# Optimization experiments

Measured on AMD Instinct MI355X. Metric: run time of the kernel, lower is better.

Reference implementation:

```python
import jax, jax.numpy as jnp
import numpy as np

B, L, D, V, O = 512, 256, 256, 100000, 1000  # L must equal D (see MaxPool1d(kernel_size=D) + squeeze)


def setup_inputs() -> dict:
    key = jax.random.key(0)
    k1, k2, k3, k4, k5 = jax.random.split(key, 5)
    input_sentence = jax.random.randint(k1, (B, L), 0, V)
    emb_weight = jax.random.normal(k2, (V, D), dtype=jnp.float32) * 0.02
    # xavier_uniform for W_b: bound = sqrt(6/(D+D))
    bound = float(np.sqrt(6.0 / (D + D)))
    W_b = jax.random.uniform(k3, (D, D), dtype=jnp.float32, minval=-bound, maxval=bound)
    lw = float(np.sqrt(1.0 / D))
    lin_w = jax.random.uniform(k4, (O, D), dtype=jnp.float32, minval=-lw, maxval=lw)
    lin_b = jax.random.uniform(k5, (O,), dtype=jnp.float32, minval=-lw, maxval=lw)
    return {"input_sentence": input_sentence, "emb_weight": emb_weight,
            "W_b": W_b, "lin_w": lin_w, "lin_b": lin_b}


def reference(input_sentence, emb_weight, W_b, lin_w, lin_b):
    # Embedding lookup: [B, L, D]
    we = emb_weight[input_sentence]
    # torch stores embeddings as [B, D, L] then re-transposes inside the co-attention;
    # net effect: C = tanh(E W_b E^T) with E = [B, L, D]  ->  C: [B, L, L]
    C = jnp.tanh(jnp.einsum('bld,de,bme->blm', we, W_b, we))
    # Dropout(p=0.5) is identity in eval mode.
    # MaxPool1d(kernel_size=D) over last axis with L == D -> max over last dim, keepdims
    max_cow = jnp.max(C, axis=-1, keepdims=True)          # [B, L, 1]
    a_q = jax.nn.softmax(max_cow, axis=1)                  # softmax over L
    # bmm(a_q^T [B,1,L], E [B,L,D]) -> [B,1,D], then squeeze dim 1
    f_w = jnp.einsum('blo,bld->bod', a_q, we)[:, 0, :]     # [B, D]
    return f_w @ lin_w.T + lin_b                           # [B, O]
```

## Files before the change

kernel.cpp:

```cpp
#include <hip/hip_runtime.h>
#include <hip/hip_bf16.h>
#include <math.h>

#define B_ 512
#define L_ 256
#define D_ 256
#define V_ 100000
#define O_ 1000

typedef __attribute__((ext_vector_type(8))) short short8;
typedef __attribute__((ext_vector_type(4))) float f32x4;

static __device__ __forceinline__ unsigned short f2bf(float f) {
    union { float f; unsigned u; } v; v.f = f;
    unsigned r = v.u + 0x7FFFu + ((v.u >> 16) & 1u);
    return (unsigned short)(r >> 16);
}
static __device__ __forceinline__ float bf2f(unsigned short u) {
    union { unsigned u; float f; } v; v.u = ((unsigned)u) << 16;
    return v.f;
}
static __device__ __forceinline__ short8 pack8(float4 a, float4 c) {
    short8 o;
    o[0] = (short)f2bf(a.x); o[1] = (short)f2bf(a.y);
    o[2] = (short)f2bf(a.z); o[3] = (short)f2bf(a.w);
    o[4] = (short)f2bf(c.x); o[5] = (short)f2bf(c.y);
    o[6] = (short)f2bf(c.z); o[7] = (short)f2bf(c.w);
    return o;
}
static __device__ __forceinline__ int fsw(int d) { return d ^ (((d >> 5) & 7) << 2); }

__global__ __launch_bounds__(256) void k_wt(const float* __restrict__ Wb,
                                            unsigned short* __restrict__ Wbf) {
    int i = blockIdx.x * 256 + threadIdx.x;
    Wbf[i] = f2bf(Wb[i]);
}

__global__ __launch_bounds__(1024, 4) void k_attn(const int* __restrict__ tok,
                                                  const float* __restrict__ emb,
                                                  const unsigned short* __restrict__ Wbf,
                                                  float* __restrict__ fw) {
    __shared__ __align__(16) char lds[163840];
    char* EsC = lds;
    float* red2    = (float*)(lds + 131072);
    float* scratch = (float*)(lds + 132096);
    float* fred    = (float*)(lds + 132160);

    int b = blockIdx.x;
    int tid = threadIdx.x;
    int wid = tid >> 6, ln = tid & 63;
    int l16 = ln & 15, gp = ln >> 4;
    bool prod = (wid < 8);
    int i0 = (prod ? wid : (wid - 8)) * 32;
    const int* tb = tok + (b << 8);

#pragma unroll
    for (int it = 0; it < 2; it++) {
        int c = it * 1024 + tid;
        int row = c >> 5, c16 = c & 31;
        const float4* src = (const float4*)(emb + ((size_t)tb[row] << 8) + (c16 << 3));
        short8 o = pack8(src[0], src[1]);
        *(short8*)(EsC + ((row << 9) | ((c16 << 4) ^ ((row & 7) << 4)))) = o;
    }

    short8 afr[8][2];
    if (prod) {
#pragma unroll
        for (int k = 0; k < 8; k++)
#pragma unroll
            for (int rf = 0; rf < 2; rf++)
                afr[k][rf] = *(const short8*)(Wbf + ((i0 + rf * 16 + l16) << 8) + k * 32 + gp * 8);
    }
    __syncthreads();

    float rmax[8];
#pragma unroll
    for (int i = 0; i < 8; i++) rmax[i] = -1e30f;

    auto P1strip = [&](int s, char* HtW) {
        f32x4 acc[2][2] = {};
#pragma unroll
        for (int k0 = 0; k0 < 256; k0 += 32) {
            int kk2 = (k0 + gp * 8) * 2;
            short8 b1[2];
#pragma unroll
            for (int cf = 0; cf < 2; cf++) {
                int jg = s * 32 + cf * 16 + l16;
                b1[cf] = *(const short8*)(EsC + ((jg << 9) | (kk2 ^ ((jg & 7) << 4))));
            }
            int ks = k0 >> 5;
            __builtin_amdgcn_s_setprio(1);
#pragma unroll
            for (int rf = 0; rf < 2; rf++)
#pragma unroll
                for (int cf = 0; cf < 2; cf++)
                    acc[rf][cf] = __builtin_amdgcn_mfma_f32_16x16x32_bf16(
                        afr[ks][rf], b1[cf], acc[rf][cf], 0, 0, 0);
            __builtin_amdgcn_s_setprio(0);
        }
#pragma unroll
        for (int rf = 0; rf < 2; rf++)
#pragma unroll
            for (int cf = 0; cf < 2; cf++) {
                int i = i0 + rf * 16 + gp * 4;
                int jl = cf * 16 + l16;
                unsigned long long pk;
                unsigned short* p = (unsigned short*)&pk;
                p[0] = f2bf(acc[rf][cf][0]);
                p[1] = f2bf(acc[rf][cf][1]);
                p[2] = f2bf(acc[rf][cf][2]);
                p[3] = f2bf(acc[rf][cf][3]);
                *(unsigned long long*)(HtW + ((jl << 9) | ((i * 2) ^ ((jl & 7) << 4)))) = pk;
            }
    };

    auto P2strip = [&](char* HtR) {
        f32x4 acc[2][2] = {};
#pragma unroll
        for (int k0 = 0; k0 < 256; k0 += 32) {
            int kk2 = (k0 + gp * 8) * 2;
            short8 b2[2];
#pragma unroll
            for (int cf = 0; cf < 2; cf++) {
                int m = cf * 16 + l16;
                b2[cf] = *(const short8*)(HtR + ((m << 9) | (kk2 ^ ((m & 7) << 4))));
            }
            int ks = k0 >> 5;
            __builtin_amdgcn_s_setprio(1);
#pragma unroll
            for (int rf = 0; rf < 2; rf++)
#pragma unroll
                for (int cf = 0; cf < 2; cf++)
                    acc[rf][cf] = __builtin_amdgcn_mfma_f32_16x16x32_bf16(
                        afr[ks][rf], b2[cf], acc[rf][cf], 0, 0, 0);
            __builtin_amdgcn_s_setprio(0);
        }
#pragma unroll
        for (int rf = 0; rf < 2; rf++)
#pragma unroll
            for (int r = 0; r < 4; r++)
                rmax[rf * 4 + r] = fmaxf(rmax[rf * 4 + r],
                                         fmaxf(acc[rf][0][r], acc[rf][1][r]));
    };

    if (prod) {
        P1strip(0, lds + 131072);
    } else {
        int t4 = tid - 512;
#pragma unroll 2
        for (int it = 0; it < 12; it++) {
            int c = it * 512 + t4;
            int row = 64 + (c >> 5), c16 = c & 31;
            const float4* src = (const float4*)(emb + ((size_t)tb[row] << 8) + (c16 << 3));
            short8 o = pack8(src[0], src[1]);
            *(short8*)(EsC + ((row << 9) | ((c16 << 4) ^ ((row & 7) << 4)))) = o;
        }
    }
    __syncthreads();

    if (!prod) {
#pragma unroll
        for (int k = 0; k < 8; k++)
#pragma unroll
            for (int rf = 0; rf < 2; rf++) {
                int l = i0 + rf * 16 + l16;
                afr[k][rf] = *(const short8*)(EsC +
                    ((l << 9) | ((k * 64 + gp * 16) ^ ((l & 7) << 4))));
            }
    }

    for (int s = 1; s < 8; s++) {
        if (prod) P1strip(s, lds + 131072 + ((s & 1) << 14));
        else      P2strip(lds + 131072 + (((s - 1) & 1) << 14));
        __syncthreads();
    }
    if (!prod) {
        P2strip(lds + 131072 + (1 << 14));
#pragma unroll
        for (int i = 0; i < 8; i++) {
            float v = rmax[i];
            v = fmaxf(v, __shfl_xor(v, 1));
            v = fmaxf(v, __shfl_xor(v, 2));
            v = fmaxf(v, __shfl_xor(v, 4));
            v = fmaxf(v, __shfl_xor(v, 8));
            rmax[i] = v;
        }
        if (l16 == 0) {
#pragma unroll
            for (int rf = 0; rf < 2; rf++)
#pragma unroll
                for (int r = 0; r < 4; r++)
                    red2[i0 + rf * 16 + gp * 4 + r] = rmax[rf * 4 + r];
        }
    }
    __syncthreads();

    float x = -1e30f;
    if (tid < 256) x = tanhf(red2[tid]);
    float mx = x;
#pragma unroll
    for (int s = 1; s < 64; s <<= 1) mx = fmaxf(mx, __shfl_xor(mx, s));
    if (ln == 0 && wid < 4) scratch[wid] = mx;
    __syncthreads();
    float bm = fmaxf(fmaxf(scratch[0], scratch[1]), fmaxf(scratch[2], scratch[3]));
    float e = (tid < 256) ? expf(x - bm) : 0.f;
    float sm = e;
#pragma unroll
    for (int s = 1; s < 64; s <<= 1) sm += __shfl_xor(sm, s);
    if (ln == 0 && wid < 4) scratch[8 + wid] = sm;
    __syncthreads();
    float tot = (scratch[8] + scratch[9]) + (scratch[10] + scratch[11]);
    if (tid < 256) red2[tid] = e / tot;
    __syncthreads();

    if (tid < 512) {
        int g = tid >> 5;
        int d0 = (tid & 31) << 3;
        float s0[8] = {0.f, 0.f, 0.f, 0.f, 0.f, 0.f, 0.f, 0.f};
        int lbase = g << 4;
#pragma unroll
        for (int li = 0; li < 16; li++) {
            int l = lbase + li;
            float aql = red2[l];
            int byt = (l << 9) | ((d0 * 2) ^ ((l & 7) << 4));
            short8 v = *(const short8*)(EsC + byt);
#pragma unroll
            for (int jj = 0; jj < 8; jj++)
                s0[jj] += aql * bf2f((unsigned short)v[jj]);
        }
        f32x4 w0, w1;
        w0[0] = s0[0]; w0[1] = s0[1]; w0[2] = s0[2]; w0[3] = s0[3];
        w1[0] = s0[4]; w1[1] = s0[5]; w1[2] = s0[6]; w1[3] = s0[7];
        *(f32x4*)(fred + g * 256 + fsw(d0)) = w0;
        *(f32x4*)(fred + g * 256 + fsw(d0 + 4)) = w1;
    }
    __syncthreads();
    if (tid < 256) {
        float f = 0.f;
        int dw = fsw(tid);
#pragma unroll
        for (int g2 = 0; g2 < 16; g2++) f += fred[g2 * 256 + dw];
        fw[(b << 8) + tid] = f;
    }
}

__global__ __launch_bounds__(256) void k_out(const float* __restrict__ fw,
                                             const float* __restrict__ lw,
                                             const float* __restrict__ lb,
                                             float* __restrict__ out) {
    __shared__ float As[32][68];
    __shared__ float Bs[64][65];
    int tid = threadIdx.x;
    int tx = tid & 15, ty = tid >> 4;
    int r0 = blockIdx.y * 32, n0 = blockIdx.x * 64;
    float acc[2][4] = {};
    for (int k0 = 0; k0 < 256; k0 += 64) {
        __syncthreads();
#pragma unroll
        for (int it = 0; it < 2; it++) {
            int idx = it * 256 + tid;
            int i = idx >> 4, k4 = (idx & 15) << 2;
            *(float4*)&As[i][k4] = *(const float4*)&fw[(r0 + i) * 256 + k0 + k4];
        }
#pragma unroll
        for (int it = 0; it < 4; it++) {
            int idx = it * 256 + tid;
            int n = idx >> 4, k4 = (idx & 15) << 2;
            int nn = n0 + n;
            float4 v = {0.f, 0.f, 0.f, 0.f};
            if (nn < O_) v = *(const float4*)&lw[(size_t)nn * 256 + k0 + k4];
            Bs[k4][n] = v.x; Bs[k4 + 1][n] = v.y; Bs[k4 + 2][n] = v.z; Bs[k4 + 3][n] = v.w;
        }
        __syncthreads();
#pragma unroll
        for (int k = 0; k < 64; k++) {
            float a0 = As[ty * 2][k], a1 = As[ty * 2 + 1][k];
            float b0 = Bs[k][tx * 4], b1 = Bs[k][tx * 4 + 1];
            float b2 = Bs[k][tx * 4 + 2], b3 = Bs[k][tx * 4 + 3];
            acc[0][0] += a0 * b0; acc[0][1] += a0 * b1; acc[0][2] += a0 * b2; acc[0][3] += a0 * b3;
            acc[1][0] += a1 * b0; acc[1][1] += a1 * b1; acc[1][2] += a1 * b2; acc[1][3] += a1 * b3;
        }
    }
#pragma unroll
    for (int i = 0; i < 2; i++)
#pragma unroll
        for (int j = 0; j < 4; j++) {
            int n = n0 + tx * 4 + j;
            if (n < O_) out[(size_t)(r0 + ty * 2 + i) * O_ + n] = acc[i][j] + lb[n];
        }
}

extern "C" void kernel_launch(void* const* d_in, const int* in_sizes, int n_in,
                              void* d_out, int out_size, void* d_ws, size_t ws_size,
                              hipStream_t stream) {
    const int* tok = (const int*)d_in[0];
    const float* emb = (const float*)d_in[1];
    const float* Wb = (const float*)d_in[2];
    const float* lw = (const float*)d_in[3];
    const float* lb = (const float*)d_in[4];
    float* out = (float*)d_out;

    char* ws = (char*)d_ws;
    unsigned short* Wbf = (unsigned short*)(ws);
    float*          fwp = (float*)(ws + 131072);

    hipLaunchKernelGGL(k_wt,   dim3(256),    dim3(256),  0, stream, Wb, Wbf);
    hipLaunchKernelGGL(k_attn, dim3(512),    dim3(1024), 0, stream, tok, emb, Wbf, fwp);
    hipLaunchKernelGGL(k_out,  dim3(16, 16), dim3(256),  0, stream, fwp, lw, lb, out);
}
```

Measured before the change: 81.26 us.

## Halve attention block to 512 threads with 64-row warps; load full K in output GEMM

```diff
diff --git a/kernel.cpp b/kernel.cpp
--- a/kernel.cpp
+++ b/kernel.cpp
@@ -36,10 +36,10 @@
     Wbf[i] = f2bf(Wb[i]);
 }
 
-__global__ __launch_bounds__(1024, 4) void k_attn(const int* __restrict__ tok,
-                                                  const float* __restrict__ emb,
-                                                  const unsigned short* __restrict__ Wbf,
-                                                  float* __restrict__ fw) {
+__global__ __launch_bounds__(512) void k_attn(const int* __restrict__ tok,
+                                              const float* __restrict__ emb,
+                                              const unsigned short* __restrict__ Wbf,
+                                              float* __restrict__ fw) {
     __shared__ __align__(16) char lds[163840];
     char* EsC = lds;
     float* red2    = (float*)(lds + 131072);
@@ -50,72 +50,35 @@
     int tid = threadIdx.x;
     int wid = tid >> 6, ln = tid & 63;
     int l16 = ln & 15, gp = ln >> 4;
-    bool prod = (wid < 8);
-    int i0 = (prod ? wid : (wid - 8)) * 32;
+    bool prod = (wid < 4);
+    int i0 = (prod ? wid : (wid - 4)) * 64;
     const int* tb = tok + (b << 8);
 
 #pragma unroll
-    for (int it = 0; it < 2; it++) {
-        int c = it * 1024 + tid;
+    for (int it = 0; it < 4; it++) {
+        int c = it * 512 + tid;
         int row = c >> 5, c16 = c & 31;
         const float4* src = (const float4*)(emb + ((size_t)tb[row] << 8) + (c16 << 3));
         short8 o = pack8(src[0], src[1]);
         *(short8*)(EsC + ((row << 9) | ((c16 << 4) ^ ((row & 7) << 4)))) = o;
     }
-
-    short8 afr[8][2];
+    __syncthreads();
+
+    short8 afr[8][4];
     if (prod) {
 #pragma unroll
         for (int k = 0; k < 8; k++)
 #pragma unroll
-            for (int rf = 0; rf < 2; rf++)
+            for (int rf = 0; rf < 4; rf++)
                 afr[k][rf] = *(const short8*)(Wbf + ((i0 + rf * 16 + l16) << 8) + k * 32 + gp * 8);
     }
-    __syncthreads();
-
-    float rmax[8];
-#pragma unroll
-    for (int i = 0; i < 8; i++) rmax[i] = -1e30f;
-
-    auto P1strip = [&](int s, char* HtW) {
-        f32x4 acc[2][2] = {};
-#pragma unroll
-        for (int k0 = 0; k0 < 256; k0 += 32) {
-            int kk2 = (k0 + gp * 8) * 2;
-            short8 b1[2];
-#pragma unroll
-            for (int cf = 0; cf < 2; cf++) {
-                int jg = s * 32 + cf * 16 + l16;
-                b1[cf] = *(const short8*)(EsC + ((jg << 9) | (kk2 ^ ((jg & 7) << 4))));
-            }
-            int ks = k0 >> 5;
-            __builtin_amdgcn_s_setprio(1);
-#pragma unroll
-            for (int rf = 0; rf < 2; rf++)
-#pragma unroll
-                for (int cf = 0; cf < 2; cf++)
-                    acc[rf][cf] = __builtin_amdgcn_mfma_f32_16x16x32_bf16(
-                        afr[ks][rf], b1[cf], acc[rf][cf], 0, 0, 0);
-            __builtin_amdgcn_s_setprio(0);
-        }
-#pragma unroll
-        for (int rf = 0; rf < 2; rf++)
-#pragma unroll
-            for (int cf = 0; cf < 2; cf++) {
-                int i = i0 + rf * 16 + gp * 4;
-                int jl = cf * 16 + l16;
-                unsigned long long pk;
-                unsigned short* p = (unsigned short*)&pk;
-                p[0] = f2bf(acc[rf][cf][0]);
-                p[1] = f2bf(acc[rf][cf][1]);
-                p[2] = f2bf(acc[rf][cf][2]);
-                p[3] = f2bf(acc[rf][cf][3]);
-                *(unsigned long long*)(HtW + ((jl << 9) | ((i * 2) ^ ((jl & 7) << 4)))) = pk;
-            }
-    };
-
-    auto P2strip = [&](char* HtR) {
-        f32x4 acc[2][2] = {};
+
+    float rmax[16];
+#pragma unroll
+    for (int i = 0; i < 16; i++) rmax[i] = -1e30f;
+
+    auto P2body = [&](char* HtR) {
+        f32x4 acc[4][2] = {};
 #pragma unroll
         for (int k0 = 0; k0 < 256; k0 += 32) {
             int kk2 = (k0 + gp * 8) * 2;
@@ -128,7 +91,7 @@
             int ks = k0 >> 5;
             __builtin_amdgcn_s_setprio(1);
 #pragma unroll
-            for (int rf = 0; rf < 2; rf++)
+            for (int rf = 0; rf < 4; rf++)
 #pragma unroll
                 for (int cf = 0; cf < 2; cf++)
                     acc[rf][cf] = __builtin_amdgcn_mfma_f32_16x16x32_bf16(
@@ -136,48 +99,82 @@
             __builtin_amdgcn_s_setprio(0);
         }
 #pragma unroll
-        for (int rf = 0; rf < 2; rf++)
+        for (int rf = 0; rf < 4; rf++)
 #pragma unroll
             for (int r = 0; r < 4; r++)
                 rmax[rf * 4 + r] = fmaxf(rmax[rf * 4 + r],
                                          fmaxf(acc[rf][0][r], acc[rf][1][r]));
     };
 
-    if (prod) {
-        P1strip(0, lds + 131072);
-    } else {
-        int t4 = tid - 512;
-#pragma unroll 2
-        for (int it = 0; it < 12; it++) {
-            int c = it * 512 + t4;
-            int row = 64 + (c >> 5), c16 = c & 31;
-            const float4* src = (const float4*)(emb + ((size_t)tb[row] << 8) + (c16 << 3));
-            short8 o = pack8(src[0], src[1]);
-            *(short8*)(EsC + ((row << 9) | ((c16 << 4) ^ ((row & 7) << 4)))) = o;
-        }
-    }
-    __syncthreads();
+    for (int s = 0; s < 8; s++) {
+        if (prod) {
+            char* HtW = lds + 131072 + ((s & 1) << 14);
+            f32x4 acc[4][2] = {};
+#pragma unroll
+            for (int k0 = 0; k0 < 256; k0 += 32) {
+                int kk2 = (k0 + gp * 8) * 2;
+                short8 b1[2];
+#pragma unroll
+                for (int cf = 0; cf < 2; cf++) {
+                    int jg = s * 32 + cf * 16 + l16;
+                    b1[cf] = *(const short8*)(EsC + ((jg << 9) | (kk2 ^ ((jg & 7) << 4))));
+                }
+                int ks = k0 >> 5;
+                __builtin_amdgcn_s_setprio(1);
+#pragma unroll
+                for (int rf = 0; rf < 4; rf++)
+#pragma unroll
+                    for (int cf = 0; cf < 2; cf++)
+                        acc[rf][cf] = __builtin_amdgcn_mfma_f32_16x16x32_bf16(
+                            afr[ks][rf], b1[cf], acc[rf][cf], 0, 0, 0);
+                __builtin_amdgcn_s_setprio(0);
+            }
+#pragma unroll
+            for (int rf = 0; rf < 4; rf++)
+#pragma unroll
+                for (int cf = 0; cf < 2; cf++) {
+                    int i = i0 + rf * 16 + gp * 4;
+                    int jl = cf * 16 + l16;
+                    unsigned long long pk;
+                    unsigned short* p = (unsigned short*)&pk;
+                    p[0] = f2bf(acc[rf][cf][0]);
+                    p[1] = f2bf(acc[rf][cf][1]);
+                    p[2] = f2bf(acc[rf][cf][2]);
+                    p[3] = f2bf(acc[rf][cf][3]);
+                    *(unsigned long long*)(HtW + ((jl << 9) | ((i * 2) ^ ((jl & 7) << 4)))) = pk;
+                }
+        } else {
+            if (s == 0) {
+                if (wid > 4) {
+#pragma unroll 4
+                    for (int it = 0; it < 32; it++) {
+                        int ch = it * 64 + ln;
+                        int rl = ch >> 5, c16 = ch & 31;
+                        int row = i0 + rl;
+                        const float4* src = (const float4*)(emb + ((size_t)tb[row] << 8) + (c16 << 3));
+                        short8 o = pack8(src[0], src[1]);
+                        *(short8*)(EsC + ((row << 9) | ((c16 << 4) ^ ((row & 7) << 4)))) = o;
+                    }
+                }
+#pragma unroll
+                for (int k = 0; k < 8; k++)
+#pragma unroll
+                    for (int rf = 0; rf < 4; rf++) {
+                        int l = i0 + rf * 16 + l16;
+                        afr[k][rf] = *(const short8*)(EsC +
+                            ((l << 9) | ((k * 64 + gp * 16) ^ ((l & 7) << 4))));
+                    }
+            } else {
+                P2body(lds + 131072 + (((s - 1) & 1) << 14));
+            }
+        }
+        __syncthreads();
+    }
 
     if (!prod) {
-#pragma unroll
-        for (int k = 0; k < 8; k++)
-#pragma unroll
-            for (int rf = 0; rf < 2; rf++) {
-                int l = i0 + rf * 16 + l16;
-                afr[k][rf] = *(const short8*)(EsC +
-                    ((l << 9) | ((k * 64 + gp * 16) ^ ((l & 7) << 4))));
-            }
-    }
-
-    for (int s = 1; s < 8; s++) {
-        if (prod) P1strip(s, lds + 131072 + ((s & 1) << 14));
-        else      P2strip(lds + 131072 + (((s - 1) & 1) << 14));
-        __syncthreads();
-    }
-    if (!prod) {
-        P2strip(lds + 131072 + (1 << 14));
-#pragma unroll
-        for (int i = 0; i < 8; i++) {
+        P2body(lds + 131072 + (1 << 14));
+#pragma unroll
+        for (int i = 0; i < 16; i++) {
             float v = rmax[i];
             v = fmaxf(v, __shfl_xor(v, 1));
             v = fmaxf(v, __shfl_xor(v, 2));
@@ -187,7 +184,7 @@
         }
         if (l16 == 0) {
 #pragma unroll
-            for (int rf = 0; rf < 2; rf++)
+            for (int rf = 0; rf < 4; rf++)
 #pragma unroll
                 for (int r = 0; r < 4; r++)
                     red2[i0 + rf * 16 + gp * 4 + r] = rmax[rf * 4 + r];
@@ -200,20 +197,24 @@
     float mx = x;
 #pragma unroll
     for (int s = 1; s < 64; s <<= 1) mx = fmaxf(mx, __shfl_xor(mx, s));
-    if (ln == 0 && wid < 4) scratch[wid] = mx;
-    __syncthreads();
-    float bm = fmaxf(fmaxf(scratch[0], scratch[1]), fmaxf(scratch[2], scratch[3]));
+    if (ln == 0) scratch[wid] = mx;
+    __syncthreads();
+    float bm = scratch[0];
+#pragma unroll
+    for (int i = 1; i < 8; i++) bm = fmaxf(bm, scratch[i]);
     float e = (tid < 256) ? expf(x - bm) : 0.f;
     float sm = e;
 #pragma unroll
     for (int s = 1; s < 64; s <<= 1) sm += __shfl_xor(sm, s);
-    if (ln == 0 && wid < 4) scratch[8 + wid] = sm;
-    __syncthreads();
-    float tot = (scratch[8] + scratch[9]) + (scratch[10] + scratch[11]);
+    if (ln == 0) scratch[8 + wid] = sm;
+    __syncthreads();
+    float tot = 0.f;
+#pragma unroll
+    for (int i = 0; i < 8; i++) tot += scratch[8 + i];
     if (tid < 256) red2[tid] = e / tot;
     __syncthreads();
 
-    if (tid < 512) {
+    {
         int g = tid >> 5;
         int d0 = (tid & 31) << 3;
         float s0[8] = {0.f, 0.f, 0.f, 0.f, 0.f, 0.f, 0.f, 0.f};
@@ -248,38 +249,34 @@
                                              const float* __restrict__ lw,
                                              const float* __restrict__ lb,
                                              float* __restrict__ out) {
-    __shared__ float As[32][68];
-    __shared__ float Bs[64][65];
+    __shared__ float BsT[256][68];
+    __shared__ float As[32][260];
     int tid = threadIdx.x;
     int tx = tid & 15, ty = tid >> 4;
     int r0 = blockIdx.y * 32, n0 = blockIdx.x * 64;
+#pragma unroll
+    for (int it = 0; it < 8; it++) {
+        int f4 = it * 256 + tid;
+        int i = f4 >> 6, kc = (f4 & 63) << 2;
+        *(float4*)&As[i][kc] = *(const float4*)&fw[(r0 + i) * 256 + kc];
+    }
+#pragma unroll
+    for (int it = 0; it < 16; it++) {
+        int f4 = it * 256 + tid;
+        int n = f4 >> 6, kc = (f4 & 63) << 2;
+        int nn = n0 + n;
+        float4 v = {0.f, 0.f, 0.f, 0.f};
+        if (nn < O_) v = *(const float4*)&lw[(size_t)nn * 256 + kc];
+        BsT[kc][n] = v.x; BsT[kc + 1][n] = v.y; BsT[kc + 2][n] = v.z; BsT[kc + 3][n] = v.w;
+    }
+    __syncthreads();
     float acc[2][4] = {};
-    for (int k0 = 0; k0 < 256; k0 += 64) {
-        __syncthreads();
-#pragma unroll
-        for (int it = 0; it < 2; it++) {
-            int idx = it * 256 + tid;
-            int i = idx >> 4, k4 = (idx & 15) << 2;
-            *(float4*)&As[i][k4] = *(const float4*)&fw[(r0 + i) * 256 + k0 + k4];
-        }
-#pragma unroll
-        for (int it = 0; it < 4; it++) {
-            int idx = it * 256 + tid;
-            int n = idx >> 4, k4 = (idx & 15) << 2;
-            int nn = n0 + n;
-            float4 v = {0.f, 0.f, 0.f, 0.f};
-            if (nn < O_) v = *(const float4*)&lw[(size_t)nn * 256 + k0 + k4];
-            Bs[k4][n] = v.x; Bs[k4 + 1][n] = v.y; Bs[k4 + 2][n] = v.z; Bs[k4 + 3][n] = v.w;
-        }
-        __syncthreads();
-#pragma unroll
-        for (int k = 0; k < 64; k++) {
-            float a0 = As[ty * 2][k], a1 = As[ty * 2 + 1][k];
-            float b0 = Bs[k][tx * 4], b1 = Bs[k][tx * 4 + 1];
-            float b2 = Bs[k][tx * 4 + 2], b3 = Bs[k][tx * 4 + 3];
-            acc[0][0] += a0 * b0; acc[0][1] += a0 * b1; acc[0][2] += a0 * b2; acc[0][3] += a0 * b3;
-            acc[1][0] += a1 * b0; acc[1][1] += a1 * b1; acc[1][2] += a1 * b2; acc[1][3] += a1 * b3;
-        }
+#pragma unroll 4
+    for (int k = 0; k < 256; k++) {
+        float4 bv = *(const float4*)&BsT[k][tx * 4];
+        float a0 = As[ty * 2][k], a1 = As[ty * 2 + 1][k];
+        acc[0][0] += a0 * bv.x; acc[0][1] += a0 * bv.y; acc[0][2] += a0 * bv.z; acc[0][3] += a0 * bv.w;
+        acc[1][0] += a1 * bv.x; acc[1][1] += a1 * bv.y; acc[1][2] += a1 * bv.z; acc[1][3] += a1 * bv.w;
     }
 #pragma unroll
     for (int i = 0; i < 2; i++)
@@ -304,7 +301,7 @@
     unsigned short* Wbf = (unsigned short*)(ws);
     float*          fwp = (float*)(ws + 131072);
 
-    hipLaunchKernelGGL(k_wt,   dim3(256),    dim3(256),  0, stream, Wb, Wbf);
-    hipLaunchKernelGGL(k_attn, dim3(512),    dim3(1024), 0, stream, tok, emb, Wbf, fwp);
-    hipLaunchKernelGGL(k_out,  dim3(16, 16), dim3(256),  0, stream, fwp, lw, lb, out);
-}
+    hipLaunchKernelGGL(k_wt,   dim3(256),    dim3(256), 0, stream, Wb, Wbf);
+    hipLaunchKernelGGL(k_attn, dim3(512),    dim3(512), 0, stream, tok, emb, Wbf, fwp);
+    hipLaunchKernelGGL(k_out,  dim3(16, 16), dim3(256), 0, stream, fwp, lw, lb, out);
+}
```

Result: faster. 79.22 us (-2.5%).
